# Kernel optimization log

Hardware: AMD Instinct MI355X
Metric: run time of the kernel (lower is better)

Reference implementation:

```python
import jax, jax.numpy as jnp
import numpy as np

GAMMA = 0.01  # matches init_kwargs gamma
BIG = 1e10    # matches tf.fill(..., 10000000000.0)


def _softmin(vals, gamma):
    # soft-min with softmin weights (my_min in the original): stable log-sum-exp
    z = -vals / gamma
    lse = jax.nn.logsumexp(z)
    return -gamma * lse, jnp.exp(z - lse)


def dtw_grad(theta, gamma):
    """Soft-DTW forward DP + backward E-recursion for one cost matrix theta [m, n].
    Returns E[1:m+1, 1:n+1] (the soft alignment / gradient matrix), shape [m, n]."""
    m, n = theta.shape

    # ---- forward DP: V[i, j] = theta[i-1, j-1] + softmin(V[i,j-1], V[i-1,j-1], V[i-1,j])
    def row_step(prev_row, theta_row):
        # prev_row = V[i-1, 0:n+1]
        def col_step(v_left, inp):
            th, v_diag, v_up = inp
            min_val, w = _softmin(jnp.stack([v_left, v_diag, v_up]), gamma)
            v = th + min_val
            return v, (v, w)
        _, (v_row, q_row) = jax.lax.scan(
            col_step, jnp.float32(BIG), (theta_row, prev_row[:-1], prev_row[1:]))
        new_row = jnp.concatenate([jnp.full((1,), BIG, theta.dtype), v_row])
        return new_row, q_row

    init_row = jnp.full((n + 1,), BIG, theta.dtype).at[0].set(0.0)  # V[0,0]=0
    _, Q_rows = jax.lax.scan(row_step, init_row, theta)  # Q_rows: (m, n, 3)

    # pad Q to (m+2, n+2, 3), Q[m+1, n+1] = [1,1,1]
    Q = (jnp.zeros((m + 2, n + 2, 3), theta.dtype)
         .at[1:m + 1, 1:n + 1].set(Q_rows)
         .at[m + 1, n + 1].set(1.0))

    # ---- backward: E[i,j] = Q[i,j+1,0]E[i,j+1] + Q[i+1,j+1,1]E[i+1,j+1] + Q[i+1,j,2]E[i+1,j]
    def brow_step(e_next, rows):
        # e_next = E[i+1, 0:n+2]; rows = (Q[i], Q[i+1]) each (n+2, 3)
        q_i, q_ip1 = rows
        # j runs n..1 (reverse order along columns)
        xs = (q_i[2:, 0][::-1],        # Q[i, j+1, 0]
              q_ip1[2:, 1][::-1],      # Q[i+1, j+1, 1]
              q_ip1[1:n + 1, 2][::-1], # Q[i+1, j, 2]
              e_next[2:][::-1],        # E[i+1, j+1]
              e_next[1:n + 1][::-1])   # E[i+1, j]

        def bcol_step(e_right, x):
            a, b, c, e1, e2 = x
            e = a * e_right + b * e1 + c * e2
            return e, e

        _, e_rev = jax.lax.scan(bcol_step, jnp.float32(0.0), xs)
        e_inner = e_rev[::-1]  # E[i, 1:n+1]
        e_row = jnp.zeros((n + 2,), theta.dtype).at[1:n + 1].set(e_inner)
        return e_row, e_inner

    e_init = jnp.zeros((n + 2,), theta.dtype).at[n + 1].set(1.0)  # E[m+1, n+1] = 1
    _, E_rev = jax.lax.scan(brow_step, e_init, (Q[m:0:-1], Q[m + 1:1:-1]))
    return E_rev[::-1]  # (m, n)


def setup_inputs() -> dict:
    key = jax.random.key(0)
    # D: batch of pairwise cost matrices, non-negative
    D = jax.random.uniform(key, (64, 256, 256), dtype=jnp.float32)
    return {"D": D}


def reference(D):
    E = jax.vmap(lambda t: dtw_grad(t, GAMMA))(D)  # (B, N, N)
    return jnp.mean(E, axis=0)
```

## Files before the change

### kernel.cpp

```cpp
#include <hip/hip_runtime.h>


#define MM 256
#define NN 256
#define R 4
#define NB 64
#define NBLK 128
#define SBIG 1.0e12f
#define K2   144.269504089f

__device__ __forceinline__ float f4get(const float4& v, int k) {
    switch (k) { case 0: return v.x; case 1: return v.y; case 2: return v.z; default: return v.w; }
}
__device__ __forceinline__ int iclamp(int x, int lo, int hi) {
    return x < lo ? lo : (x > hi ? hi : x);
}

template<bool REV>
__device__ __forceinline__ void run_dp(const float* __restrict__ th,
                                       float* __restrict__ Vp)
{
    const int L = threadIdx.x;

    float vprev[R];
    #pragma unroll
    for (int r = 0; r < R; ++r) vprev[r] = SBIG;
    float4 rec = make_float4(SBIG, SBIG, SBIG, SBIG);
    float prevW = SBIG;
    float4 botV4 = make_float4(SBIG, SBIG, SBIG, SBIG);
    float4 thB[3][R];
    #pragma unroll
    for (int p = 0; p < 3; ++p)
        #pragma unroll
        for (int r = 0; r < R; ++r) thB[p][r] = make_float4(0.f, 0.f, 0.f, 0.f);

    auto body = [&](const int LD, const int CU, const int m) {
        const int g = m - L;
        const int gl = iclamp(g + 2, 0, 63);
        #pragma unroll
        for (int r = 0; r < R; ++r) {
            const int vr = 4 * L + r;
            if (REV) {
                const float4 t = *(const float4*)(th + (255 - vr) * NN + (252 - 4 * gl));
                thB[LD][r] = make_float4(t.w, t.z, t.y, t.x);
            } else {
                thB[LD][r] = *(const float4*)(th + vr * NN + 4 * gl);
            }
        }
        if ((unsigned)g <= 63u) {
            const float4 topV = rec;
            const float vd0 = (g == 0) ? ((L == 0) ? 0.0f : SBIG) : prevW;
            float vbuf[R][4];
            #pragma unroll
            for (int cc = 0; cc < 4; ++cc) {
                float vu = f4get(topV, cc);
                float vd = (cc == 0) ? vd0 : f4get(topV, cc - 1);
                #pragma unroll
                for (int r = 0; r < R; ++r) {
                    const float vl = vprev[r];
                    const float mn = fminf(vl, fminf(vd, vu));
                    const float el = exp2f(mn - vl);
                    const float ed = exp2f(mn - vd);
                    const float eu = exp2f(mn - vu);
                    const float ss = el + ed + eu;
                    const float a  = mn - log2f(ss);
                    const float v  = fmaf(f4get(thB[CU][r], cc), K2, a);
                    vbuf[r][cc] = v;
                    vd = vl;
                    vu = v;
                    vprev[r] = v;
                }
            }
            botV4 = make_float4(vbuf[R - 1][0], vbuf[R - 1][1], vbuf[R - 1][2], vbuf[R - 1][3]);
            #pragma unroll
            for (int r = 0; r < R; ++r) {
                const int vr = 4 * L + r;
                if (REV)
                    *(float4*)(Vp + (255 - vr) * NN + (252 - 4 * g)) =
                        make_float4(vbuf[r][3], vbuf[r][2], vbuf[r][1], vbuf[r][0]);
                else
                    *(float4*)(Vp + vr * NN + 4 * g) =
                        make_float4(vbuf[r][0], vbuf[r][1], vbuf[r][2], vbuf[r][3]);
            }
        }
        float4 nr;
        nr.x = __shfl_up(botV4.x, 1);
        nr.y = __shfl_up(botV4.y, 1);
        nr.z = __shfl_up(botV4.z, 1);
        nr.w = __shfl_up(botV4.w, 1);
        prevW = rec.w;
        if (L == 0) nr = make_float4(SBIG, SBIG, SBIG, SBIG);
        rec = nr;
    };
    for (int k = 0; k < 129; k += 3) {
        body(0, 1, k - 2);
        body(1, 2, k - 1);
        body(2, 0, k);
    }
}

__global__ __launch_bounds__(64, 1) void dtw_fb(
    const float* __restrict__ D,
    float* __restrict__ out,
    float* __restrict__ ws)
{
    const int blk = blockIdx.x;
    const bool rev = blk >= NB;
    const int b = rev ? blk - NB : blk;
    const float* __restrict__ th = D + (size_t)b * (MM * NN);
    float* __restrict__ Fp = ws + (size_t)b * (MM * NN);
    float* __restrict__ Bp = ws + (size_t)(NB + b) * (MM * NN);
    unsigned* ctr = (unsigned*)(ws + (size_t)2 * NB * (MM * NN));

    if (rev) run_dp<true >(th, Bp);
    else     run_dp<false>(th, Fp);

    __threadfence();
    if (threadIdx.x == 0)
        __hip_atomic_fetch_add(ctr, 1u, __ATOMIC_ACQ_REL, __HIP_MEMORY_SCOPE_AGENT);
    unsigned cnt;
    do {
        cnt = __hip_atomic_load(ctr, __ATOMIC_ACQUIRE, __HIP_MEMORY_SCOPE_AGENT);
        if (cnt < NBLK) __builtin_amdgcn_s_sleep(2);
    } while (cnt < NBLK);
    __builtin_amdgcn_fence(__ATOMIC_ACQUIRE, "agent");

    {
        const int t = threadIdx.x;
        const int row = 2 * blk + (t >> 5);
        const int cb  = 4 * (t & 31);
        const size_t off0 = (size_t)row * NN + cb;
        const size_t off1 = off0 + 128;
        float4 acc0 = make_float4(0.f, 0.f, 0.f, 0.f);
        float4 acc1 = make_float4(0.f, 0.f, 0.f, 0.f);
        for (int p = 0; p < NB; ++p) {
            const float* __restrict__ thp = D + (size_t)p * (MM * NN);
            const float* __restrict__ fp  = ws + (size_t)p * (MM * NN);
            const float* __restrict__ bp  = ws + (size_t)(NB + p) * (MM * NN);
            const float Ft = fp[MM * NN - 1];
            const float4 t0 = *(const float4*)(thp + off0);
            const float4 f0 = *(const float4*)(fp + off0);
            const float4 b0 = *(const float4*)(bp + off0);
            acc0.x += exp2f(fmaf(t0.x, K2, (Ft - f0.x) - b0.x));
            acc0.y += exp2f(fmaf(t0.y, K2, (Ft - f0.y) - b0.y));
            acc0.z += exp2f(fmaf(t0.z, K2, (Ft - f0.z) - b0.z));
            acc0.w += exp2f(fmaf(t0.w, K2, (Ft - f0.w) - b0.w));
            const float4 t1 = *(const float4*)(thp + off1);
            const float4 f1 = *(const float4*)(fp + off1);
            const float4 b1 = *(const float4*)(bp + off1);
            acc1.x += exp2f(fmaf(t1.x, K2, (Ft - f1.x) - b1.x));
            acc1.y += exp2f(fmaf(t1.y, K2, (Ft - f1.y) - b1.y));
            acc1.z += exp2f(fmaf(t1.z, K2, (Ft - f1.z) - b1.z));
            acc1.w += exp2f(fmaf(t1.w, K2, (Ft - f1.w) - b1.w));
        }
        const float inv = 1.0f / (float)NB;
        *(float4*)(out + off0) =
            make_float4(acc0.x * inv, acc0.y * inv, acc0.z * inv, acc0.w * inv);
        *(float4*)(out + off1) =
            make_float4(acc1.x * inv, acc1.y * inv, acc1.z * inv, acc1.w * inv);
    }
}

extern "C" void kernel_launch(void* const* d_in, const int* in_sizes, int n_in,
                              void* d_out, int out_size, void* d_ws, size_t ws_size,
                              hipStream_t stream) {
    const float* D = (const float*)d_in[0];
    float* out = (float*)d_out;
    float* ws = (float*)d_ws;

    hipMemsetAsync(ws + (size_t)2 * NB * (MM * NN), 0, sizeof(unsigned), stream);
    dtw_fb<<<dim3(NBLK), dim3(64), 0, stream>>>(D, out, ws);
}
```

Baseline: 266.3 us.

## Run soft-DTW DP in linear (exp) domain with fp64 and per-lane block exponent scaling

Replaces the log-domain softmin (three exp2 plus one log2 per cell) with a linear-domain recurrence: each cell becomes a product of exp(-theta/gamma) with the sum of three neighbour values, carried in fp64 with a per-lane shared exponent that is rescaled by ldexp each step. The log value is recovered cheaply from the double's exponent bits plus a single log2 of the mantissa. The goal is to cut transcendental work on the serial critical path. The theta loads are also issued through inline asm with an explicit waitcnt. The cost is fp64 arithmetic (slow on some parts), shuffling doubles plus the scale, and possible precision or range edge cases.

```diff
diff --git a/kernel.cpp b/kernel.cpp
--- a/kernel.cpp
+++ b/kernel.cpp
@@ -6,14 +6,21 @@
 #define R 4
 #define NB 64
 #define NBLK 128
-#define SBIG 1.0e12f
 #define K2   144.269504089f
-
-__device__ __forceinline__ float f4get(const float4& v, int k) {
-    switch (k) { case 0: return v.x; case 1: return v.y; case 2: return v.z; default: return v.w; }
-}
+#define TB64 1700
+
+typedef float f32x4 __attribute__((ext_vector_type(4)));
+
 __device__ __forceinline__ int iclamp(int x, int lo, int hi) {
     return x < lo ? lo : (x > hi ? hi : x);
+}
+__device__ __forceinline__ int imax(int a, int b) { return a > b ? a : b; }
+__device__ __forceinline__ int bexp64(double x) {
+    return (int)(((unsigned long long)__double_as_longlong(x) >> 52) & 2047u);
+}
+__device__ __forceinline__ int rexp64(double x, int d) {
+    const int e = bexp64(x);
+    return e == 0 ? 0 : e + d;
 }
 
 template<bool REV>
@@ -22,17 +29,20 @@
 {
     const int L = threadIdx.x;
 
-    float vprev[R];
+    double up[R];
+    double rcv[4];
+    double bot[4];
+    double prevW = 0.0;
     #pragma unroll
-    for (int r = 0; r < R; ++r) vprev[r] = SBIG;
-    float4 rec = make_float4(SBIG, SBIG, SBIG, SBIG);
-    float prevW = SBIG;
-    float4 botV4 = make_float4(SBIG, SBIG, SBIG, SBIG);
-    float4 thB[3][R];
+    for (int r = 0; r < R; ++r) up[r] = 0.0;
+    #pragma unroll
+    for (int j = 0; j < 4; ++j) { rcv[j] = 0.0; bot[j] = 0.0; }
+    int S = 0, recS = 0, prevWS = 0;
+    f32x4 thB[3][R];
     #pragma unroll
     for (int p = 0; p < 3; ++p)
         #pragma unroll
-        for (int r = 0; r < R; ++r) thB[p][r] = make_float4(0.f, 0.f, 0.f, 0.f);
+        for (int r = 0; r < R; ++r) thB[p][r] = (f32x4)0.0f;
 
     auto body = [&](const int LD, const int CU, const int m) {
         const int g = m - L;
@@ -40,57 +50,84 @@
         #pragma unroll
         for (int r = 0; r < R; ++r) {
             const int vr = 4 * L + r;
-            if (REV) {
-                const float4 t = *(const float4*)(th + (255 - vr) * NN + (252 - 4 * gl));
-                thB[LD][r] = make_float4(t.w, t.z, t.y, t.x);
-            } else {
-                thB[LD][r] = *(const float4*)(th + vr * NN + 4 * gl);
+            const float* addr = REV ? (th + (255 - vr) * NN + (252 - 4 * gl))
+                                    : (th + vr * NN + 4 * gl);
+            asm volatile("global_load_dwordx4 %0, %1, off"
+                         : "=v"(thB[LD][r]) : "v"(addr));
+        }
+        if ((unsigned)g <= 63u) {
+            asm volatile("s_waitcnt vmcnt(8)" ::: "memory");
+            __builtin_amdgcn_sched_barrier(0);
+
+            const int drec = S - recS, dpw = S - prevWS;
+            int em = bexp64(up[0]);
+            em = imax(em, bexp64(up[1])); em = imax(em, bexp64(up[2]));
+            em = imax(em, bexp64(up[3]));
+            em = imax(em, rexp64(rcv[0], drec)); em = imax(em, rexp64(rcv[1], drec));
+            em = imax(em, rexp64(rcv[2], drec)); em = imax(em, rexp64(rcv[3], drec));
+            em = imax(em, rexp64(prevW, dpw));
+            if (g == 0 && L == 0) em = imax(em, 1023 + S);
+            const int k0 = em - TB64;
+            S -= k0;
+            #pragma unroll
+            for (int j = 0; j < 4; ++j) rcv[j] = ldexp(rcv[j], drec - k0);
+            prevW = ldexp(prevW, dpw - k0);
+            #pragma unroll
+            for (int r = 0; r < R; ++r) up[r] = ldexp(up[r], -k0);
+            const double ud0 = (g == 0) ? ((L == 0) ? ldexp(1.0, S) : 0.0)
+                                        : prevW;
+
+            float vbuf[R][4];
+            #pragma unroll
+            for (int cc = 0; cc < 4; ++cc) {
+                double pdc[R];
+                #pragma unroll
+                for (int r = 0; r < R; ++r) {
+                    const float thv = thB[CU][r][REV ? 3 - cc : cc];
+                    const float f  = -K2 * thv;
+                    const float fi = rintf(f);
+                    pdc[r] = ldexp((double)exp2f(f - fi), (int)fi);
+                }
+                double pre[R];
+                pre[0] = ((cc == 0) ? ud0 : rcv[cc - 1]) + up[0];
+                #pragma unroll
+                for (int r = 1; r < R; ++r) pre[r] = up[r - 1] + up[r];
+                double vu = rcv[cc];
+                #pragma unroll
+                for (int r = 0; r < R; ++r) {
+                    const double un = pdc[r] * (pre[r] + vu);
+                    const long long ub = __double_as_longlong(un);
+                    const int ef = (int)(((unsigned long long)ub >> 52) & 2047u);
+                    const double mant = __longlong_as_double(
+                        (ub & 0x000FFFFFFFFFFFFFLL) | 0x3FF0000000000000LL);
+                    vbuf[r][cc] = (ef == 0)
+                        ? __builtin_inff()
+                        : ((float)(S - (ef - 1023)) - log2f((float)mant));
+                    if (r == R - 1) bot[cc] = un;
+                    vu = un; up[r] = un;
+                }
+            }
+            recS = S;
+            #pragma unroll
+            for (int r = 0; r < R; ++r) {
+                const int vr = 4 * L + r;
+                if (REV) {
+                    f32x4 sv = {vbuf[r][3], vbuf[r][2], vbuf[r][1], vbuf[r][0]};
+                    *(f32x4*)(Vp + (255 - vr) * NN + (252 - 4 * g)) = sv;
+                } else {
+                    f32x4 sv = {vbuf[r][0], vbuf[r][1], vbuf[r][2], vbuf[r][3]};
+                    *(f32x4*)(Vp + vr * NN + 4 * g) = sv;
+                }
             }
         }
-        if ((unsigned)g <= 63u) {
-            const float4 topV = rec;
-            const float vd0 = (g == 0) ? ((L == 0) ? 0.0f : SBIG) : prevW;
-            float vbuf[R][4];
-            #pragma unroll
-            for (int cc = 0; cc < 4; ++cc) {
-                float vu = f4get(topV, cc);
-                float vd = (cc == 0) ? vd0 : f4get(topV, cc - 1);
-                #pragma unroll
-                for (int r = 0; r < R; ++r) {
-                    const float vl = vprev[r];
-                    const float mn = fminf(vl, fminf(vd, vu));
-                    const float el = exp2f(mn - vl);
-                    const float ed = exp2f(mn - vd);
-                    const float eu = exp2f(mn - vu);
-                    const float ss = el + ed + eu;
-                    const float a  = mn - log2f(ss);
-                    const float v  = fmaf(f4get(thB[CU][r], cc), K2, a);
-                    vbuf[r][cc] = v;
-                    vd = vl;
-                    vu = v;
-                    vprev[r] = v;
-                }
-            }
-            botV4 = make_float4(vbuf[R - 1][0], vbuf[R - 1][1], vbuf[R - 1][2], vbuf[R - 1][3]);
-            #pragma unroll
-            for (int r = 0; r < R; ++r) {
-                const int vr = 4 * L + r;
-                if (REV)
-                    *(float4*)(Vp + (255 - vr) * NN + (252 - 4 * g)) =
-                        make_float4(vbuf[r][3], vbuf[r][2], vbuf[r][1], vbuf[r][0]);
-                else
-                    *(float4*)(Vp + vr * NN + 4 * g) =
-                        make_float4(vbuf[r][0], vbuf[r][1], vbuf[r][2], vbuf[r][3]);
-            }
-        }
-        float4 nr;
-        nr.x = __shfl_up(botV4.x, 1);
-        nr.y = __shfl_up(botV4.y, 1);
-        nr.z = __shfl_up(botV4.z, 1);
-        nr.w = __shfl_up(botV4.w, 1);
-        prevW = rec.w;
-        if (L == 0) nr = make_float4(SBIG, SBIG, SBIG, SBIG);
-        rec = nr;
+        const double nb0 = __shfl_up(bot[0], 1);
+        const double nb1 = __shfl_up(bot[1], 1);
+        const double nb2 = __shfl_up(bot[2], 1);
+        const double nb3 = __shfl_up(bot[3], 1);
+        const int   nbS = __shfl_up(S, 1);
+        prevW = rcv[3]; prevWS = recS;
+        rcv[0] = nb0; rcv[1] = nb1; rcv[2] = nb2; rcv[3] = nb3; recS = nbS;
+        if (L == 0) { rcv[0] = rcv[1] = rcv[2] = rcv[3] = 0.0; recS = S; }
     };
     for (int k = 0; k < 129; k += 3) {
         body(0, 1, k - 2);
```

After: 271.9 us. 1.02x slower.
